# Kernel optimization log

Hardware: AMD Instinct MI355X
Metric: run time of the kernel (lower is better)

The kernel has to match this reference:

```python
import jax, jax.numpy as jnp
import numpy as np

D = 128
EPS = 1e-5

def group_norm1(x, gamma, beta):
    # GroupNorm with num_groups=1 over channel dim of [N, C]
    mu = jnp.mean(x, axis=-1, keepdims=True)
    var = jnp.mean(jnp.square(x - mu), axis=-1, keepdims=True)
    xhat = (x - mu) * jax.lax.rsqrt(var + EPS)
    return xhat * gamma + beta

def setup_inputs() -> dict:
    key = jax.random.key(0)
    ks = jax.random.split(key, 12)
    N_ctx, N_tgt, E = 40000, 40000, 640000
    s = 0.09  # ~1/sqrt(128) weight scale
    inp = {
        'context_feat': jax.random.normal(ks[0], (N_ctx, D), jnp.float32),
        'target_feat': jax.random.normal(ks[1], (N_tgt, D), jnp.float32),
        'context_pose': jax.random.normal(ks[2], (N_ctx, 4), jnp.float32),
        'target_pose': jax.random.normal(ks[3], (N_tgt, 4), jnp.float32),
        'W_input': s * jax.random.normal(ks[4], (D, D), jnp.float32),
        'W_rp': 0.5 * jax.random.normal(ks[5], (4, D), jnp.float32),
        'b_rp': jnp.zeros((D,), jnp.float32),
        'W_c1': s * jax.random.normal(ks[6], (2 * D, D), jnp.float32),
        'g_c1': jnp.ones((D,), jnp.float32),
        'b_c1': jnp.zeros((D,), jnp.float32),
        'W_c2': s * jax.random.normal(ks[7], (D, D), jnp.float32),
        'g_n': jnp.ones((D,), jnp.float32),
        'b_n': jnp.zeros((D,), jnp.float32),
        'W_m1': s * jax.random.normal(ks[8], (D, D), jnp.float32),
        'g_m1': jnp.ones((D,), jnp.float32),
        'bm1': jnp.zeros((D,), jnp.float32),
        'W_m2': s * jax.random.normal(ks[9], (D, D), jnp.float32),
        'g_m2': jnp.ones((D,), jnp.float32),
        'bm2': jnp.zeros((D,), jnp.float32),
        'hi': jax.random.randint(ks[10], (E,), 0, N_ctx, jnp.int32),
        'wi': jax.random.randint(ks[11], (E,), 0, N_tgt, jnp.int32),
    }
    return inp

def reference(context_feat, target_feat, context_pose, target_pose,
              W_input, W_rp, b_rp, W_c1, g_c1, b_c1, W_c2,
              g_n, b_n, W_m1, g_m1, bm1, W_m2, g_m2, bm2, hi, wi):
    # relpose: Linear(4,128) + ReLU on relative pose of each (context, target) edge
    dist_feat = context_pose[hi] - target_pose[wi]                 # [E, 4]
    dist_feat = jax.nn.relu(dist_feat @ W_rp + b_rp)               # [E, 128]
    # ctx: Linear(256,128,GN,ReLU) -> Linear(128,128, no bias)
    ctx = jnp.concatenate([context_feat[hi], dist_feat], axis=-1)  # [E, 256]
    ctx = jax.nn.relu(group_norm1(ctx @ W_c1, g_c1, b_c1))
    ctx = ctx @ W_c2                                               # [E, 128]
    # input linear + index_add scatter into targets
    tf = target_feat @ W_input                                     # [N_tgt, 128]
    tf = tf + jax.ops.segment_sum(ctx, wi, num_segments=target_feat.shape[0])
    tf = jax.nn.relu(group_norm1(tf, g_n, b_n))
    # mlp: Linear(GN,ReLU) -> Linear(GN, no act)
    tf = jax.nn.relu(group_norm1(tf @ W_m1, g_m1, bm1))
    tf = group_norm1(tf @ W_m2, g_m2, bm2)
    # residual + relu
    return jax.nn.relu(tf + target_feat)
```

## Files before the change

kernel.cpp:

```cpp
#include <hip/hip_runtime.h>

#define D 128
#define EPSV 1e-5f

typedef __attribute__((ext_vector_type(8))) __bf16 bf16x8;
typedef __attribute__((ext_vector_type(4))) float f32x4;

__device__ __forceinline__ ushort f2bf(float x) {
  unsigned u = __float_as_uint(x);
  u += 0x7fffu + ((u >> 16) & 1u);
  return (ushort)(u >> 16);
}
__device__ __forceinline__ unsigned cvtpk(float lo, float hi) {
  unsigned r;
  asm("v_cvt_pk_bf16_f32 %0, %1, %2" : "=v"(r) : "v"(lo), "v"(hi));
  return r;
}
__device__ __forceinline__ int yidx(int row, int col) {
  return row * 128 + (col ^ ((row & 7) << 3));
}

__global__ void k_cvt(const float* __restrict__ Wc1, const float* __restrict__ Wc2,
                      ushort* __restrict__ WT1, ushort* __restrict__ WT2) {
  int i = blockIdx.x * 256 + threadIdx.x;
  if (i < 128 * 256) {
    int n = i >> 8, k = i & 255;
    WT1[i] = f2bf(Wc1[k * 128 + n]);
  } else {
    int j = i - 128 * 256;
    if (j < 128 * 128) {
      int n = j >> 7, k = j & 127;
      WT2[j] = f2bf(Wc2[k * 128 + n]);
    }
  }
}

__global__ __launch_bounds__(256, 3) void k_edge(
    const float* __restrict__ cfeat,
    const float* __restrict__ cpose, const float* __restrict__ tpose,
    const float* __restrict__ Wrp, const float* __restrict__ brp,
    const float* __restrict__ gc1, const float* __restrict__ bc1,
    const ushort* __restrict__ WT1, const ushort* __restrict__ WT2,
    const int* __restrict__ hi, const int* __restrict__ wi,
    float* __restrict__ acc, int E) {
  __shared__ ushort Wbuf[2][4096];
  __shared__ ushort Ybuf[128 * 128];
  __shared__ float gnbuf[2][128][2];
  __shared__ int wl[128];

  const int t = threadIdx.x;
  const int lane = t & 63;
  const int wv = t >> 6;
  const int wm = wv >> 1, wn = wv & 1;
  const int s = lane & 15, g = lane >> 4;
  const int e0 = blockIdx.x * 128;

  auto stage = [&](int c, int nb) {
    const ushort* Wt = (c < 8) ? WT1 : WT2;
    const int koff = (c < 8 ? c : c - 8) * 32;
    const int krow = (c < 8) ? 256 : 128;
    const int col = t & 127, g0 = t >> 7;
#pragma unroll
    for (int v = 0; v < 2; ++v) {
      const int gg = g0 + v * 2;
      const ushort* src = Wt + (size_t)col * krow + koff + gg * 8;
      ushort* dst = &Wbuf[nb][(gg * 128 + col) * 8];
      __builtin_amdgcn_global_load_lds(
          (const __attribute__((address_space(1))) void*)src,
          (__attribute__((address_space(3))) void*)dst, 16, 0, 0);
    }
  };

  stage(0, 0);
  if (t < 128) wl[t] = wi[min(e0 + t, E - 1)];

  int hl[4];
#pragma unroll
  for (int m = 0; m < 4; ++m)
    hl[m] = hi[min(e0 + wm * 64 + m * 16 + s, E - 1)];

  {
    const int e = t >> 1;
    const int jh = (t & 1) * 64;
    const int ge = min(e0 + e, E - 1);
    const int h = hi[ge], w = wi[ge];
    float4 cp = *(const float4*)(cpose + (size_t)h * 4);
    float4 tp = *(const float4*)(tpose + (size_t)w * 4);
    const float d0 = cp.x - tp.x, d1 = cp.y - tp.y;
    const float d2 = cp.z - tp.z, d3 = cp.w - tp.w;
#pragma unroll
    for (int q = 0; q < 16; ++q) {
      const int j = jh + q * 4;
      float4 b  = *(const float4*)(brp + j);
      float4 w0 = *(const float4*)(Wrp + j);
      float4 w1 = *(const float4*)(Wrp + D + j);
      float4 w2 = *(const float4*)(Wrp + 2 * D + j);
      float4 w3 = *(const float4*)(Wrp + 3 * D + j);
      float r0 = fmaxf(b.x + d0 * w0.x + d1 * w1.x + d2 * w2.x + d3 * w3.x, 0.f);
      float r1 = fmaxf(b.y + d0 * w0.y + d1 * w1.y + d2 * w2.y + d3 * w3.y, 0.f);
      float r2 = fmaxf(b.z + d0 * w0.z + d1 * w1.z + d2 * w2.z + d3 * w3.z, 0.f);
      float r3 = fmaxf(b.w + d0 * w0.w + d1 * w1.w + d2 * w2.w + d3 * w3.w, 0.f);
      *(uint2*)&Ybuf[yidx(e, j)] = make_uint2(cvtpk(r0, r1), cvtpk(r2, r3));
    }
  }
  __syncthreads();

  f32x4 acc1[4][4];
#pragma unroll
  for (int m = 0; m < 4; ++m)
#pragma unroll
    for (int n = 0; n < 4; ++n) acc1[m][n] = (f32x4){0.f, 0.f, 0.f, 0.f};

  for (int kc = 0; kc < 8; ++kc) {
    const int nb = kc & 1;
    stage(kc + 1, nb ^ 1);
    bf16x8 a[4];
    if (kc < 4) {
#pragma unroll
      for (int m = 0; m < 4; ++m) {
        const float* src = cfeat + (size_t)hl[m] * D + kc * 32 + g * 8;
        float4 f0 = *(const float4*)src;
        float4 f1 = *(const float4*)(src + 4);
        union { uint4 u; bf16x8 v; } cv;
        cv.u.x = cvtpk(f0.x, f0.y); cv.u.y = cvtpk(f0.z, f0.w);
        cv.u.z = cvtpk(f1.x, f1.y); cv.u.w = cvtpk(f1.z, f1.w);
        a[m] = cv.v;
      }
    } else {
#pragma unroll
      for (int m = 0; m < 4; ++m)
        a[m] = *(const bf16x8*)
            &Ybuf[yidx(wm * 64 + m * 16 + s, (kc - 4) * 32 + g * 8)];
    }
#pragma unroll
    for (int n = 0; n < 4; ++n) {
      bf16x8 b = *(const bf16x8*)
          &Wbuf[nb][(g * 128 + wn * 64 + n * 16 + s) * 8];
#pragma unroll
      for (int m = 0; m < 4; ++m)
        acc1[m][n] =
            __builtin_amdgcn_mfma_f32_16x16x32_bf16(a[m], b, acc1[m][n], 0, 0, 0);
    }
    __syncthreads();
  }

#pragma unroll
  for (int m = 0; m < 4; ++m) {
#pragma unroll
    for (int reg = 0; reg < 4; ++reg) {
      float p1 = acc1[m][0][reg] + acc1[m][1][reg] + acc1[m][2][reg] +
                 acc1[m][3][reg];
      float p2 = acc1[m][0][reg] * acc1[m][0][reg] +
                 acc1[m][1][reg] * acc1[m][1][reg] +
                 acc1[m][2][reg] * acc1[m][2][reg] +
                 acc1[m][3][reg] * acc1[m][3][reg];
#pragma unroll
      for (int msk = 1; msk < 16; msk <<= 1) {
        p1 += __shfl_xor(p1, msk, 64);
        p2 += __shfl_xor(p2, msk, 64);
      }
      if (s == 0) {
        const int row = wm * 64 + m * 16 + g * 4 + reg;
        *(float2*)&gnbuf[wn][row][0] = make_float2(p1, p2);
      }
    }
  }
  __syncthreads();

  {
    float gcl[4], bcl[4];
#pragma unroll
    for (int n = 0; n < 4; ++n) {
      gcl[n] = gc1[wn * 64 + n * 16 + s];
      bcl[n] = bc1[wn * 64 + n * 16 + s];
    }
#pragma unroll
    for (int m = 0; m < 4; ++m) {
#pragma unroll
      for (int reg = 0; reg < 4; ++reg) {
        const int row = wm * 64 + m * 16 + g * 4 + reg;
        float2 q0 = *(const float2*)&gnbuf[0][row][0];
        float2 q1 = *(const float2*)&gnbuf[1][row][0];
        const float mean = (q0.x + q1.x) * (1.f / 128.f);
        const float var = (q0.y + q1.y) * (1.f / 128.f) - mean * mean;
        const float rstd = rsqrtf(var + EPSV);
#pragma unroll
        for (int n = 0; n < 4; ++n) {
          float y = fmaxf((acc1[m][n][reg] - mean) * rstd * gcl[n] + bcl[n], 0.f);
          Ybuf[yidx(row, wn * 64 + n * 16 + s)] = (ushort)cvtpk(y, y);
        }
      }
    }
  }
  __syncthreads();

  f32x4 acc2[4][4];
#pragma unroll
  for (int m = 0; m < 4; ++m)
#pragma unroll
    for (int n = 0; n < 4; ++n) acc2[m][n] = (f32x4){0.f, 0.f, 0.f, 0.f};

  for (int kc = 0; kc < 4; ++kc) {
    const int c = 8 + kc;
    const int nb = c & 1;
    if (c < 11) stage(c + 1, nb ^ 1);
    bf16x8 a[4];
#pragma unroll
    for (int m = 0; m < 4; ++m)
      a[m] = *(const bf16x8*)
          &Ybuf[yidx(wm * 64 + m * 16 + s, kc * 32 + g * 8)];
#pragma unroll
    for (int n = 0; n < 4; ++n) {
      bf16x8 b = *(const bf16x8*)
          &Wbuf[nb][(g * 128 + wn * 64 + n * 16 + s) * 8];
#pragma unroll
      for (int m = 0; m < 4; ++m)
        acc2[m][n] =
            __builtin_amdgcn_mfma_f32_16x16x32_bf16(a[m], b, acc2[m][n], 0, 0, 0);
    }
    if (kc < 3) __syncthreads();
  }

#pragma unroll
  for (int m = 0; m < 4; ++m) {
#pragma unroll
    for (int reg = 0; reg < 4; ++reg) {
      const int rl = wm * 64 + m * 16 + g * 4 + reg;
      if (e0 + rl < E) {
        const int w = wl[rl];
        float* base = acc + (size_t)w * D + wn * 64 + s;
#pragma unroll
        for (int n = 0; n < 4; ++n)
          unsafeAtomicAdd(base + n * 16, acc2[m][n][reg]);
      }
    }
  }
}

__device__ __forceinline__ void reduce16(float& a, float& b) {
#pragma unroll
  for (int w = 1; w < 16; w <<= 1) {
    a += __shfl_xor(a, w, 64);
    b += __shfl_xor(b, w, 64);
  }
}

__global__ __launch_bounds__(256, 2) void k_input(
    const float* __restrict__ tfeat, const float* __restrict__ Wi,
    float* __restrict__ acc, int N) {
  __shared__ float Wbuf[64][132];
  __shared__ float xt[64][132];
  const int t = threadIdx.x;
  const int r = t >> 4, s = t & 15, j0 = s * 8;
  const int row0 = blockIdx.x * 64;

  for (int idx = t; idx < 64 * 32; idx += 256) {
    int rr = idx >> 5, c4 = idx & 31;
    int grow = row0 + rr;
    float4 v = make_float4(0.f, 0.f, 0.f, 0.f);
    if (grow < N) v = *(const float4*)(tfeat + (size_t)grow * D + c4 * 4);
    *(float4*)&xt[rr][c4 * 4] = v;
  }

  float a[4][8] = {};
  for (int kc = 0; kc < 2; ++kc) {
    __syncthreads();
    for (int idx = t; idx < 64 * 32; idx += 256) {
      int kk = idx >> 5, c4 = idx & 31;
      *(float4*)&Wbuf[kk][c4 * 4] =
          *(const float4*)(Wi + (size_t)(kc * 64 + kk) * D + c4 * 4);
    }
    __syncthreads();
#pragma unroll 4
    for (int kk = 0; kk < 64; ++kk) {
      float4 w0 = *(const float4*)&Wbuf[kk][j0];
      float4 w1 = *(const float4*)&Wbuf[kk][j0 + 4];
#pragma unroll
      for (int i = 0; i < 4; ++i) {
        float xv = xt[r + 16 * i][kc * 64 + kk];
        a[i][0] += xv * w0.x; a[i][1] += xv * w0.y;
        a[i][2] += xv * w0.z; a[i][3] += xv * w0.w;
        a[i][4] += xv * w1.x; a[i][5] += xv * w1.y;
        a[i][6] += xv * w1.z; a[i][7] += xv * w1.w;
      }
    }
  }
#pragma unroll
  for (int i = 0; i < 4; ++i) {
    int row = row0 + r + 16 * i;
    if (row < N) {
      *(float4*)(acc + (size_t)row * D + j0) =
          make_float4(a[i][0], a[i][1], a[i][2], a[i][3]);
      *(float4*)(acc + (size_t)row * D + j0 + 4) =
          make_float4(a[i][4], a[i][5], a[i][6], a[i][7]);
    }
  }
}

__global__ __launch_bounds__(256, 2) void k_node(
    const float* __restrict__ tfeat,
    const float* __restrict__ gn, const float* __restrict__ bn,
    const float* __restrict__ Wm1, const float* __restrict__ gm1,
    const float* __restrict__ bm1,
    const float* __restrict__ Wm2, const float* __restrict__ gm2,
    const float* __restrict__ bm2,
    float* __restrict__ acc, int N) {
  __shared__ float Wbuf[64][132];
  __shared__ float xt[64][132];
  const int t = threadIdx.x;
  const int r = t >> 4, s = t & 15, j0 = s * 8;
  const int row0 = blockIdx.x * 64;

  auto stageW = [&](const float* W, int kc) {
    for (int idx = t; idx < 64 * 32; idx += 256) {
      int kk = idx >> 5, c4 = idx & 31;
      *(float4*)&Wbuf[kk][c4 * 4] =
          *(const float4*)(W + (size_t)(kc * 64 + kk) * D + c4 * 4);
    }
  };
  auto gemm = [&](float (&a)[4][8], int kc) {
#pragma unroll 4
    for (int kk = 0; kk < 64; ++kk) {
      float4 w0 = *(const float4*)&Wbuf[kk][j0];
      float4 w1 = *(const float4*)&Wbuf[kk][j0 + 4];
#pragma unroll
      for (int i = 0; i < 4; ++i) {
        float xv = xt[r + 16 * i][kc * 64 + kk];
        a[i][0] += xv * w0.x; a[i][1] += xv * w0.y;
        a[i][2] += xv * w0.z; a[i][3] += xv * w0.w;
        a[i][4] += xv * w1.x; a[i][5] += xv * w1.y;
        a[i][6] += xv * w1.z; a[i][7] += xv * w1.w;
      }
    }
  };

  {
    float gv[8], bv[8];
#pragma unroll
    for (int m = 0; m < 8; ++m) { gv[m] = gn[j0 + m]; bv[m] = bn[j0 + m]; }
#pragma unroll
    for (int i = 0; i < 4; ++i) {
      int row = row0 + r + 16 * i;
      float v[8] = {};
      if (row < N) {
        float4 v0 = *(const float4*)(acc + (size_t)row * D + j0);
        float4 v1 = *(const float4*)(acc + (size_t)row * D + j0 + 4);
        v[0] = v0.x; v[1] = v0.y; v[2] = v0.z; v[3] = v0.w;
        v[4] = v1.x; v[5] = v1.y; v[6] = v1.z; v[7] = v1.w;
      }
      float s1 = 0.f, s2 = 0.f;
#pragma unroll
      for (int m = 0; m < 8; ++m) { s1 += v[m]; s2 += v[m] * v[m]; }
      reduce16(s1, s2);
      float mean = s1 * (1.f / 128.f);
      float var = s2 * (1.f / 128.f) - mean * mean;
      float rstd = rsqrtf(var + EPSV);
#pragma unroll
      for (int m = 0; m < 8; ++m)
        xt[r + 16 * i][j0 + m] = fmaxf((v[m] - mean) * rstd * gv[m] + bv[m], 0.f);
    }
  }

  float a[4][8] = {};
  for (int kc = 0; kc < 2; ++kc) {
    __syncthreads();
    stageW(Wm1, kc);
    __syncthreads();
    gemm(a, kc);
  }
  __syncthreads();
  {
    float gv[8], bv[8];
#pragma unroll
    for (int m = 0; m < 8; ++m) { gv[m] = gm1[j0 + m]; bv[m] = bm1[j0 + m]; }
#pragma unroll
    for (int i = 0; i < 4; ++i) {
      float s1 = 0.f, s2 = 0.f;
#pragma unroll
      for (int m = 0; m < 8; ++m) { s1 += a[i][m]; s2 += a[i][m] * a[i][m]; }
      reduce16(s1, s2);
      float mean = s1 * (1.f / 128.f);
      float var = s2 * (1.f / 128.f) - mean * mean;
      float rstd = rsqrtf(var + EPSV);
#pragma unroll
      for (int m = 0; m < 8; ++m)
        xt[r + 16 * i][j0 + m] =
            fmaxf((a[i][m] - mean) * rstd * gv[m] + bv[m], 0.f);
    }
  }

  float a2[4][8] = {};
  for (int kc = 0; kc < 2; ++kc) {
    __syncthreads();
    stageW(Wm2, kc);
    __syncthreads();
    gemm(a2, kc);
  }
  {
    float gv[8], bv[8];
#pragma unroll
    for (int m = 0; m < 8; ++m) { gv[m] = gm2[j0 + m]; bv[m] = bm2[j0 + m]; }
#pragma unroll
    for (int i = 0; i < 4; ++i) {
      int row = row0 + r + 16 * i;
      float s1 = 0.f, s2 = 0.f;
#pragma unroll
      for (int m = 0; m < 8; ++m) { s1 += a2[i][m]; s2 += a2[i][m] * a2[i][m]; }
      reduce16(s1, s2);
      float mean = s1 * (1.f / 128.f);
      float var = s2 * (1.f / 128.f) - mean * mean;
      float rstd = rsqrtf(var + EPSV);
      if (row < N) {
        float o[8];
#pragma unroll
        for (int m = 0; m < 8; ++m) {
          float x = (a2[i][m] - mean) * rstd * gv[m] + bv[m];
          o[m] = fmaxf(x + tfeat[(size_t)row * D + j0 + m], 0.f);
        }
        *(float4*)(acc + (size_t)row * D + j0) =
            make_float4(o[0], o[1], o[2], o[3]);
        *(float4*)(acc + (size_t)row * D + j0 + 4) =
            make_float4(o[4], o[5], o[6], o[7]);
      }
    }
  }
}

extern "C" void kernel_launch(void* const* d_in, const int* in_sizes, int n_in,
                              void* d_out, int out_size, void* d_ws,
                              size_t ws_size, hipStream_t stream) {
  const float* cfeat = (const float*)d_in[0];
  const float* tfeat = (const float*)d_in[1];
  const float* cpose = (const float*)d_in[2];
  const float* tpose = (const float*)d_in[3];
  const float* Wi    = (const float*)d_in[4];
  const float* Wrp   = (const float*)d_in[5];
  const float* brp   = (const float*)d_in[6];
  const float* Wc1   = (const float*)d_in[7];
  const float* gc1   = (const float*)d_in[8];
  const float* bc1   = (const float*)d_in[9];
  const float* Wc2   = (const float*)d_in[10];
  const float* gn    = (const float*)d_in[11];
  const float* bn    = (const float*)d_in[12];
  const float* Wm1   = (const float*)d_in[13];
  const float* gm1   = (const float*)d_in[14];
  const float* bm1   = (const float*)d_in[15];
  const float* Wm2   = (const float*)d_in[16];
  const float* gm2   = (const float*)d_in[17];
  const float* bm2   = (const float*)d_in[18];
  const int* hi      = (const int*)d_in[19];
  const int* wi      = (const int*)d_in[20];

  const int N = in_sizes[1] / D;
  const int E = in_sizes[19];
  float* out = (float*)d_out;

  ushort* WT1 = (ushort*)d_ws;
  ushort* WT2 = WT1 + 128 * 256;

  const int nbN = (N + 63) / 64;
  const int nbE = (E + 127) / 128;

  k_cvt<<<192, 256, 0, stream>>>(Wc1, Wc2, WT1, WT2);
  k_input<<<nbN, 256, 0, stream>>>(tfeat, Wi, out, N);
  k_edge<<<nbE, 256, 0, stream>>>(cfeat, cpose, tpose, Wrp, brp, gc1, bc1,
                                  WT1, WT2, hi, wi, out, E);
  k_node<<<nbN, 256, 0, stream>>>(tfeat, gn, bn, Wm1, gm1, bm1, Wm2, gm2, bm2,
                                  out, N);
}
```

Measured before the change: 444.8 us.

## Read weight fragments from global in MFMA layout and pre-convert context features to bf16

Weights are converted once into a fragment-major bf16 layout so each lane reads its MFMA B operand straight from global/L2. This drops the LDS double-buffered staging and most per-chunk barriers. Context features are converted to bf16 in a separate pass when workspace allows, which halves the gathered bytes per edge. Launch bounds rise to 4 blocks per CU since LDS use shrinks. The trade-off is that the B operands now depend on cache hits instead of LDS reuse, plus an extra conversion kernel pass over the context features.

Result: slower. 476.3 us (+7.1%).

```diff
diff --git a/kernel.cpp b/kernel.cpp
--- a/kernel.cpp
+++ b/kernel.cpp
@@ -21,29 +21,42 @@
 }
 
 __global__ void k_cvt(const float* __restrict__ Wc1, const float* __restrict__ Wc2,
-                      ushort* __restrict__ WT1, ushort* __restrict__ WT2) {
+                      ushort* __restrict__ WF1, ushort* __restrict__ WF2) {
+  int o = blockIdx.x * 256 + threadIdx.x;
+  if (o < 32768) {
+    int j = o & 7, col = (o >> 3) & 127, gg = (o >> 10) & 3, kc = o >> 12;
+    WF1[o] = f2bf(Wc1[(kc * 32 + gg * 8 + j) * 128 + col]);
+  } else {
+    int o2 = o - 32768;
+    if (o2 < 16384) {
+      int j = o2 & 7, col = (o2 >> 3) & 127, gg = (o2 >> 10) & 3, kc = o2 >> 12;
+      WF2[o2] = f2bf(Wc2[(kc * 32 + gg * 8 + j) * 128 + col]);
+    }
+  }
+}
+
+__global__ void k_cvtf(const float* __restrict__ cf, ushort* __restrict__ cb,
+                       int n8) {
   int i = blockIdx.x * 256 + threadIdx.x;
-  if (i < 128 * 256) {
-    int n = i >> 8, k = i & 255;
-    WT1[i] = f2bf(Wc1[k * 128 + n]);
-  } else {
-    int j = i - 128 * 256;
-    if (j < 128 * 128) {
-      int n = j >> 7, k = j & 127;
-      WT2[j] = f2bf(Wc2[k * 128 + n]);
-    }
-  }
-}
-
-__global__ __launch_bounds__(256, 3) void k_edge(
-    const float* __restrict__ cfeat,
+  if (i < n8) {
+    float4 f0 = *(const float4*)(cf + (size_t)i * 8);
+    float4 f1 = *(const float4*)(cf + (size_t)i * 8 + 4);
+    uint4 p;
+    p.x = cvtpk(f0.x, f0.y); p.y = cvtpk(f0.z, f0.w);
+    p.z = cvtpk(f1.x, f1.y); p.w = cvtpk(f1.z, f1.w);
+    *(uint4*)(cb + (size_t)i * 8) = p;
+  }
+}
+
+template <bool BF16CF>
+__global__ __launch_bounds__(256, 4) void k_edge(
+    const float* __restrict__ cfeat, const ushort* __restrict__ cfb,
     const float* __restrict__ cpose, const float* __restrict__ tpose,
     const float* __restrict__ Wrp, const float* __restrict__ brp,
     const float* __restrict__ gc1, const float* __restrict__ bc1,
-    const ushort* __restrict__ WT1, const ushort* __restrict__ WT2,
+    const ushort* __restrict__ WF1, const ushort* __restrict__ WF2,
     const int* __restrict__ hi, const int* __restrict__ wi,
     float* __restrict__ acc, int E) {
-  __shared__ ushort Wbuf[2][4096];
   __shared__ ushort Ybuf[128 * 128];
   __shared__ float gnbuf[2][128][2];
   __shared__ int wl[128];
@@ -55,23 +68,6 @@
   const int s = lane & 15, g = lane >> 4;
   const int e0 = blockIdx.x * 128;
 
-  auto stage = [&](int c, int nb) {
-    const ushort* Wt = (c < 8) ? WT1 : WT2;
-    const int koff = (c < 8 ? c : c - 8) * 32;
-    const int krow = (c < 8) ? 256 : 128;
-    const int col = t & 127, g0 = t >> 7;
-#pragma unroll
-    for (int v = 0; v < 2; ++v) {
-      const int gg = g0 + v * 2;
-      const ushort* src = Wt + (size_t)col * krow + koff + gg * 8;
-      ushort* dst = &Wbuf[nb][(gg * 128 + col) * 8];
-      __builtin_amdgcn_global_load_lds(
-          (const __attribute__((address_space(1))) void*)src,
-          (__attribute__((address_space(3))) void*)dst, 16, 0, 0);
-    }
-  };
-
-  stage(0, 0);
   if (t < 128) wl[t] = wi[min(e0 + t, E - 1)];
 
   int hl[4];
@@ -103,7 +99,10 @@
       *(uint2*)&Ybuf[yidx(e, j)] = make_uint2(cvtpk(r0, r1), cvtpk(r2, r3));
     }
   }
-  __syncthreads();
+
+  auto bfrag = [&](const ushort* WF, int kc, int n) {
+    return *(const bf16x8*)&WF[(((kc * 4 + g) * 128) + wn * 64 + n * 16 + s) * 8];
+  };
 
   f32x4 acc1[4][4];
 #pragma unroll
@@ -111,11 +110,13 @@
 #pragma unroll
     for (int n = 0; n < 4; ++n) acc1[m][n] = (f32x4){0.f, 0.f, 0.f, 0.f};
 
-  for (int kc = 0; kc < 8; ++kc) {
-    const int nb = kc & 1;
-    stage(kc + 1, nb ^ 1);
+  for (int kc = 0; kc < 4; ++kc) {
     bf16x8 a[4];
-    if (kc < 4) {
+    if (BF16CF) {
+#pragma unroll
+      for (int m = 0; m < 4; ++m)
+        a[m] = *(const bf16x8*)(cfb + (size_t)hl[m] * D + kc * 32 + g * 8);
+    } else {
 #pragma unroll
       for (int m = 0; m < 4; ++m) {
         const float* src = cfeat + (size_t)hl[m] * D + kc * 32 + g * 8;
@@ -126,22 +127,33 @@
         cv.u.z = cvtpk(f1.x, f1.y); cv.u.w = cvtpk(f1.z, f1.w);
         a[m] = cv.v;
       }
-    } else {
-#pragma unroll
-      for (int m = 0; m < 4; ++m)
-        a[m] = *(const bf16x8*)
-            &Ybuf[yidx(wm * 64 + m * 16 + s, (kc - 4) * 32 + g * 8)];
     }
 #pragma unroll
     for (int n = 0; n < 4; ++n) {
-      bf16x8 b = *(const bf16x8*)
-          &Wbuf[nb][(g * 128 + wn * 64 + n * 16 + s) * 8];
+      bf16x8 b = bfrag(WF1, kc, n);
 #pragma unroll
       for (int m = 0; m < 4; ++m)
         acc1[m][n] =
             __builtin_amdgcn_mfma_f32_16x16x32_bf16(a[m], b, acc1[m][n], 0, 0, 0);
     }
-    __syncthreads();
+  }
+
+  __syncthreads();
+
+  for (int kc = 4; kc < 8; ++kc) {
+    bf16x8 a[4];
+#pragma unroll
+    for (int m = 0; m < 4; ++m)
+      a[m] = *(const bf16x8*)
+          &Ybuf[yidx(wm * 64 + m * 16 + s, (kc - 4) * 32 + g * 8)];
+#pragma unroll
+    for (int n = 0; n < 4; ++n) {
+      bf16x8 b = bfrag(WF1, kc, n);
+#pragma unroll
+      for (int m = 0; m < 4; ++m)
+        acc1[m][n] =
+            __builtin_amdgcn_mfma_f32_16x16x32_bf16(a[m], b, acc1[m][n], 0, 0, 0);
+    }
   }
 
 #pragma unroll
@@ -201,24 +213,18 @@
     for (int n = 0; n < 4; ++n) acc2[m][n] = (f32x4){0.f, 0.f, 0.f, 0.f};
 
   for (int kc = 0; kc < 4; ++kc) {
-    const int c = 8 + kc;
-    const int nb = c & 1;
-    if (c < 11) stage(c + 1, nb ^ 1);
     bf16x8 a[4];
 #pragma unroll
     for (int m = 0; m < 4; ++m)
-      a[m] = *(const bf16x8*)
-          &Ybuf[yidx(wm * 64 + m * 16 + s, kc * 32 + g * 8)];
+      a[m] = *(const bf16x8*)&Ybuf[yidx(wm * 64 + m * 16 + s, kc * 32 + g * 8)];
 #pragma unroll
     for (int n = 0; n < 4; ++n) {
-      bf16x8 b = *(const bf16x8*)
-          &Wbuf[nb][(g * 128 + wn * 64 + n * 16 + s) * 8];
+      bf16x8 b = bfrag(WF2, kc, n);
 #pragma unroll
       for (int m = 0; m < 4; ++m)
         acc2[m][n] =
             __builtin_amdgcn_mfma_f32_16x16x32_bf16(a[m], b, acc2[m][n], 0, 0, 0);
     }
-    if (kc < 3) __syncthreads();
   }
 
 #pragma unroll
@@ -453,18 +459,27 @@
 
   const int N = in_sizes[1] / D;
   const int E = in_sizes[19];
+  const int CFE = in_sizes[0];
   float* out = (float*)d_out;
 
-  ushort* WT1 = (ushort*)d_ws;
-  ushort* WT2 = WT1 + 128 * 256;
+  uint8_t* ws = (uint8_t*)d_ws;
+  ushort* WF1 = (ushort*)ws;
+  ushort* WF2 = (ushort*)(ws + 65536);
+  ushort* cfb = (ushort*)(ws + 98304);
+  const bool bf16cf = ws_size >= 98304 + (size_t)CFE * 2;
 
   const int nbN = (N + 63) / 64;
   const int nbE = (E + 127) / 128;
 
-  k_cvt<<<192, 256, 0, stream>>>(Wc1, Wc2, WT1, WT2);
+  k_cvt<<<192, 256, 0, stream>>>(Wc1, Wc2, WF1, WF2);
+  if (bf16cf) k_cvtf<<<(CFE / 8 + 255) / 256, 256, 0, stream>>>(cfeat, cfb, CFE / 8);
   k_input<<<nbN, 256, 0, stream>>>(tfeat, Wi, out, N);
-  k_edge<<<nbE, 256, 0, stream>>>(cfeat, cpose, tpose, Wrp, brp, gc1, bc1,
-                                  WT1, WT2, hi, wi, out, E);
+  if (bf16cf)
+    k_edge<true><<<nbE, 256, 0, stream>>>(cfeat, cfb, cpose, tpose, Wrp, brp,
+                                          gc1, bc1, WF1, WF2, hi, wi, out, E);
+  else
+    k_edge<false><<<nbE, 256, 0, stream>>>(cfeat, cfb, cpose, tpose, Wrp, brp,
+                                           gc1, bc1, WF1, WF2, hi, wi, out, E);
   k_node<<<nbN, 256, 0, stream>>>(tfeat, gn, bn, Wm1, gm1, bm1, Wm2, gm2, bm2,
                                   out, N);
 }
```
